# Kernel optimization log

Hardware: AMD Instinct MI355X
Metric: run time of the kernel (lower is better)

## Reference

```python
import jax, jax.numpy as jnp
import numpy as np


def setup_inputs() -> dict:
    key = jax.random.key(0)
    k1, k2 = jax.random.split(key)
    q_embed = jax.random.normal(k1, (1000, 1024), dtype=jnp.float32)      # (V, D)
    conv_feat = jax.random.normal(k2, (64, 1024, 800), dtype=jnp.float32)  # (B, D, T)
    return {"q_embed": q_embed, "conv_feat": conv_feat}


def reference(q_embed, conv_feat):
    # sim_scores: (B, V, T) = q_embed (V, D) @ conv_feat (B, D, T), no scaling
    sim_scores = jnp.einsum('vd,bdt->bvt', q_embed, conv_feat)
    attention_weights = jax.nn.softmax(sim_scores, axis=2)  # over T
    # context: (B, V, D) = weights (B, V, T) @ conv_feat^T (B, T, D)
    context_vector = jnp.einsum('bvt,bdt->bvd', attention_weights, conv_feat)
    return (context_vector, attention_weights)
```

## Files before the change

### kernel.cpp

```cpp
#include <hip/hip_runtime.h>
#include <hip/hip_bf16.h>

typedef short bf16x8 __attribute__((ext_vector_type(8)));
typedef float f32x4 __attribute__((ext_vector_type(4)));

#define NV 1000
#define ND 1024
#define NT 800
#define NB 64

__device__ inline unsigned short f32_bf16(float f) {
    unsigned u = __builtin_bit_cast(unsigned, f);
    return (unsigned short)((u + 0x7FFFu + ((u >> 16) & 1u)) >> 16);
}
__device__ inline void split_bf16(float f, unsigned short& h, unsigned short& l) {
    unsigned u = __builtin_bit_cast(unsigned, f);
    unsigned hb = (u + 0x7FFFu + ((u >> 16) & 1u)) >> 16;
    h = (unsigned short)hb;
    float hf = __builtin_bit_cast(float, hb << 16);
    float lf = f - hf;
    unsigned ul = __builtin_bit_cast(unsigned, lf);
    l = (unsigned short)((ul + 0x7FFFu + ((ul >> 16) & 1u)) >> 16);
}

__device__ inline void gload16(const void* g, void* l) {
    __builtin_amdgcn_global_load_lds(
        (const __attribute__((address_space(1))) unsigned int*)g,
        (__attribute__((address_space(3))) unsigned int*)l, 16, 0, 0);
}

__global__ __launch_bounds__(256) void prep_q(const float* __restrict__ Q,
                                              unsigned short* __restrict__ Qh,
                                              unsigned short* __restrict__ Ql) {
    int idx = blockIdx.x * 256 + threadIdx.x;
    int row = idx >> 8;
    int c4 = (idx & 255) << 2;
    float4 f = make_float4(0.f, 0.f, 0.f, 0.f);
    if (row < NV) f = *(const float4*)(Q + (size_t)row * ND + c4);
    unsigned short h0,h1,h2,h3,l0,l1,l2,l3;
    split_bf16(f.x,h0,l0); split_bf16(f.y,h1,l1);
    split_bf16(f.z,h2,l2); split_bf16(f.w,h3,l3);
    *(ushort4*)(Qh + (size_t)row * ND + c4) = make_ushort4(h0,h1,h2,h3);
    *(ushort4*)(Ql + (size_t)row * ND + c4) = make_ushort4(l0,l1,l2,l3);
}

__global__ __launch_bounds__(256) void prep_c(const float* __restrict__ C,
                                              unsigned short* __restrict__ Cth,
                                              unsigned short* __restrict__ Ctl,
                                              unsigned short* __restrict__ Cbf,
                                              int writeCbf) {
    const int dt = blockIdx.x;
    const int tt = blockIdx.y;
    const int b  = blockIdx.z;
    const int tid = threadIdx.x;
    __shared__ float T[64][33];
    const float* Cb = C + (size_t)b * ND * NT;
    const int d0 = dt * 64, t0 = tt * 32;
#pragma unroll
    for (int r = 0; r < 2; ++r) {
        int idx = r * 256 + tid;
        int row = idx >> 3;
        int c4 = (idx & 7) << 2;
        float4 f = *(const float4*)(Cb + (size_t)(d0 + row) * NT + t0 + c4);
        T[row][c4 + 0] = f.x; T[row][c4 + 1] = f.y;
        T[row][c4 + 2] = f.z; T[row][c4 + 3] = f.w;
        if (writeCbf) {
            *(ushort4*)(Cbf + ((size_t)b * ND + d0 + row) * NT + t0 + c4) =
                make_ushort4(f32_bf16(f.x), f32_bf16(f.y), f32_bf16(f.z), f32_bf16(f.w));
        }
    }
    __syncthreads();
#pragma unroll
    for (int r = 0; r < 2; ++r) {
        int idx = r * 256 + tid;
        int trow = idx >> 4;
        int dc = (idx & 15) << 2;
        unsigned short h[4], l[4];
#pragma unroll
        for (int j = 0; j < 4; ++j) split_bf16(T[dc + j][trow], h[j], l[j]);
        size_t o = ((size_t)b * NT + t0 + trow) * ND + d0 + dc;
        *(ushort4*)(Cth + o) = make_ushort4(h[0],h[1],h[2],h[3]);
        *(ushort4*)(Ctl + o) = make_ushort4(l[0],l[1],l[2],l[3]);
    }
}

__global__ __launch_bounds__(256) void gemm1_kernel(const unsigned short* __restrict__ Qh,
                                                    const unsigned short* __restrict__ Ql,
                                                    const unsigned short* __restrict__ Cth,
                                                    const unsigned short* __restrict__ Ctl,
                                                    float* __restrict__ S) {
    const int h = blockIdx.x;
    const int L = (h & 7) * 320 + (h >> 3);
    const int bm = L & 7;
    const int rest = L >> 3;
    const int bn = rest % 5;
    const int b  = rest / 5;

    const int tid = threadIdx.x;
    const int lane = tid & 63;
    const int w = tid >> 6;
    const int wr = w >> 1, wc = w & 1;

    __shared__ unsigned short lds[2][18432];

    const int v0 = bm * 128, t0 = bn * 160;
    const unsigned short* Agh = Qh + (size_t)v0 * ND;
    const unsigned short* Agl = Ql + (size_t)v0 * ND;
    const unsigned short* Bgh = Cth + ((size_t)b * NT + t0) * ND;
    const unsigned short* Bgl = Ctl + ((size_t)b * NT + t0) * ND;

    f32x4 acc[4][5];
#pragma unroll
    for (int i = 0; i < 4; ++i)
#pragma unroll
        for (int j = 0; j < 5; ++j) acc[i][j] = (f32x4){0.f, 0.f, 0.f, 0.f};

    const int srow = lane >> 2;
    const int sslot = lane & 3;
    const int swz = (sslot ^ (srow & 3) ^ ((srow >> 2) & 3)) << 3;
    const int g = lane >> 4, rl = lane & 15;
    const int sx = (g ^ (rl & 3) ^ ((rl >> 2) & 3)) << 4;

#define G1_STAGE(K0, BUF)                                                     \
    {                                                                         \
        unsigned short* Lb = lds[BUF];                                        \
        for (int i = w; i < 8; i += 4) {                                      \
            int row = i * 16 + srow;                                          \
            gload16(Agh + (size_t)row * ND + swz + (K0), Lb + i * 512);       \
            gload16(Agl + (size_t)row * ND + swz + (K0), Lb + 4096 + i * 512);\
        }                                                                     \
        for (int i = w; i < 10; i += 4) {                                     \
            int row = i * 16 + srow;                                          \
            gload16(Bgh + (size_t)row * ND + swz + (K0), Lb + 8192 + i * 512);\
            gload16(Bgl + (size_t)row * ND + swz + (K0), Lb + 13312 + i * 512);\
        }                                                                     \
    }

#define G1_COMPUTE(BUF)                                                       \
    {                                                                         \
        const char* Lb = (const char*)lds[BUF];                               \
        bf16x8 ah[4], al[4], bh[5], bl[5];                                    \
        _Pragma("unroll")                                                     \
        for (int mf = 0; mf < 4; ++mf) {                                      \
            int off = (wr * 64 + mf * 16 + rl) * 64 + sx;                     \
            ah[mf] = *(const bf16x8*)(Lb + off);                              \
            al[mf] = *(const bf16x8*)(Lb + 8192 + off);                       \
        }                                                                     \
        _Pragma("unroll")                                                     \
        for (int nf = 0; nf < 5; ++nf) {                                      \
            int off = (wc * 80 + nf * 16 + rl) * 64 + sx;                     \
            bh[nf] = *(const bf16x8*)(Lb + 16384 + off);                      \
            bl[nf] = *(const bf16x8*)(Lb + 26624 + off);                      \
        }                                                                     \
        _Pragma("unroll")                                                     \
        for (int mf = 0; mf < 4; ++mf)                                        \
            _Pragma("unroll")                                                 \
            for (int nf = 0; nf < 5; ++nf) {                                  \
                acc[mf][nf] = __builtin_amdgcn_mfma_f32_16x16x32_bf16(ah[mf], bh[nf], acc[mf][nf], 0, 0, 0); \
                acc[mf][nf] = __builtin_amdgcn_mfma_f32_16x16x32_bf16(ah[mf], bl[nf], acc[mf][nf], 0, 0, 0); \
                acc[mf][nf] = __builtin_amdgcn_mfma_f32_16x16x32_bf16(al[mf], bh[nf], acc[mf][nf], 0, 0, 0); \
            }                                                                 \
    }

    G1_STAGE(0, 0);
    __syncthreads();
    int cur = 0;
    for (int t = 0; t < 31; ++t) {
        G1_STAGE((t + 1) * 32, cur ^ 1);
        G1_COMPUTE(cur);
        __syncthreads();
        cur ^= 1;
    }
    G1_COMPUTE(cur);

    float* Sb = S + (size_t)b * NV * NT;
#pragma unroll
    for (int mf = 0; mf < 4; ++mf) {
#pragma unroll
        for (int nf = 0; nf < 5; ++nf) {
#pragma unroll
            for (int r = 0; r < 4; ++r) {
                int v = v0 + wr * 64 + mf * 16 + g * 4 + r;
                int t = t0 + wc * 80 + nf * 16 + rl;
                if (v < NV) Sb[(size_t)v * NT + t] = acc[mf][nf][r];
            }
        }
    }
#undef G1_STAGE
#undef G1_COMPUTE
}

__global__ __launch_bounds__(256) void softmax_kernel(float* __restrict__ S,
                                                      unsigned short* __restrict__ Wbf,
                                                      int writeWbf) {
    const int row = blockIdx.x * 4 + (threadIdx.x >> 6);
    const int lane = threadIdx.x & 63;
    float* p = S + (size_t)row * NT;
    unsigned short* pw = Wbf + (size_t)row * NT;
    float v[13];
    float m = -INFINITY;
#pragma unroll
    for (int i = 0; i < 13; ++i) {
        int t = i * 64 + lane;
        v[i] = (t < NT) ? p[t] : -INFINITY;
        m = fmaxf(m, v[i]);
    }
#pragma unroll
    for (int off = 32; off; off >>= 1) m = fmaxf(m, __shfl_xor(m, off));
    float s = 0.f;
#pragma unroll
    for (int i = 0; i < 13; ++i) {
        int t = i * 64 + lane;
        float e = (t < NT) ? __expf(v[i] - m) : 0.f;
        v[i] = e;
        s += e;
    }
#pragma unroll
    for (int off = 32; off; off >>= 1) s += __shfl_xor(s, off);
    const float inv = 1.0f / s;
#pragma unroll
    for (int i = 0; i < 13; ++i) {
        int t = i * 64 + lane;
        if (t < NT) {
            float wv = v[i] * inv;
            p[t] = wv;
            if (writeWbf) pw[t] = f32_bf16(wv);
        }
    }
}

__global__ __launch_bounds__(512) void gemm2_fast(const unsigned short* __restrict__ Wbf,
                                                  const unsigned short* __restrict__ Cbf,
                                                  float* __restrict__ O) {
    const int h = blockIdx.x;
    const int L = (h & 7) * 128 + (h >> 3);
    const int b  = L >> 4;
    const int bm = (L >> 2) & 3;
    const int bn = L & 3;
    const int tid = threadIdx.x;
    const int lane = tid & 63;
    const int w = tid >> 6;
    const int wr = w >> 2, wc = w & 3;

    __shared__ unsigned short lds[2][16384];

    const int v0 = bm * 256, d0 = bn * 256;
    const unsigned short* Ag = Wbf + (size_t)b * NV * NT;
    const unsigned short* Bg = Cbf + ((size_t)b * ND + d0) * NT;

    f32x4 acc[8][4];
#pragma unroll
    for (int i = 0; i < 8; ++i)
#pragma unroll
        for (int j = 0; j < 4; ++j) acc[i][j] = (f32x4){0.f, 0.f, 0.f, 0.f};

    const int srow = lane >> 2;
    const int sslot = lane & 3;
    const int swz = (sslot ^ (srow & 3) ^ ((srow >> 2) & 3)) << 3;
    const int g = lane >> 4, rl = lane & 15;
    const int sx = (g ^ (rl & 3) ^ ((rl >> 2) & 3)) << 4;

#define G2_STAGE(K0, BUF)                                                     \
    {                                                                         \
        unsigned short* Lb = lds[BUF];                                        \
        for (int i = w; i < 16; i += 8) {                                     \
            int row = i * 16 + srow;                                          \
            int vrow = v0 + row; if (vrow > NV - 1) vrow = NV - 1;            \
            gload16(Ag + (size_t)vrow * NT + swz + (K0), Lb + i * 512);       \
            gload16(Bg + (size_t)row * NT + swz + (K0), Lb + 8192 + i * 512); \
        }                                                                     \
    }

#define G2_COMPUTE(BUF)                                                       \
    {                                                                         \
        const char* Lb = (const char*)lds[BUF];                               \
        bf16x8 a[8], bq[4];                                                   \
        _Pragma("unroll")                                                     \
        for (int mf = 0; mf < 8; ++mf) {                                      \
            int off = (wr * 128 + mf * 16 + rl) * 64 + sx;                    \
            a[mf] = *(const bf16x8*)(Lb + off);                               \
        }                                                                     \
        _Pragma("unroll")                                                     \
        for (int nf = 0; nf < 4; ++nf) {                                      \
            int off = (wc * 64 + nf * 16 + rl) * 64 + sx;                     \
            bq[nf] = *(const bf16x8*)(Lb + 16384 + off);                      \
        }                                                                     \
        _Pragma("unroll")                                                     \
        for (int mf = 0; mf < 8; ++mf)                                        \
            _Pragma("unroll")                                                 \
            for (int nf = 0; nf < 4; ++nf)                                    \
                acc[mf][nf] = __builtin_amdgcn_mfma_f32_16x16x32_bf16(a[mf], bq[nf], acc[mf][nf], 0, 0, 0); \
    }

    G2_STAGE(0, 0);
    __syncthreads();
    int cur = 0;
    for (int t = 0; t < 24; ++t) {
        G2_STAGE((t + 1) * 32, cur ^ 1);
        G2_COMPUTE(cur);
        __syncthreads();
        cur ^= 1;
    }
    G2_COMPUTE(cur);

    float* Ob = O + (size_t)b * NV * ND;
#pragma unroll
    for (int mf = 0; mf < 8; ++mf) {
#pragma unroll
        for (int nf = 0; nf < 4; ++nf) {
#pragma unroll
            for (int r = 0; r < 4; ++r) {
                int v = v0 + wr * 128 + mf * 16 + g * 4 + r;
                int d = d0 + wc * 64 + nf * 16 + rl;
                if (v < NV) Ob[(size_t)v * ND + d] = acc[mf][nf][r];
            }
        }
    }
#undef G2_STAGE
#undef G2_COMPUTE
}

__global__ __launch_bounds__(256) void gemm2_mid(const unsigned short* __restrict__ Wbf,
                                                 const float* __restrict__ C,
                                                 float* __restrict__ O) {
    const int h = blockIdx.x;
    const int L = (h & 7) * 512 + (h >> 3);
    const int bm = L & 7;
    const int bn = (L >> 3) & 7;
    const int b  = L >> 6;
    const int tid = threadIdx.x;
    const int lane = tid & 63;
    const int w = tid >> 6;
    const int wr = w >> 1, wc = w & 1;

    __shared__ unsigned short As[128 * 32];
    __shared__ unsigned short Bs[128][40];

    const int v0 = bm * 128, d0 = bn * 128;
    const unsigned short* Ag = Wbf + (size_t)b * NV * NT;
    const float* Cb = C + (size_t)b * ND * NT;

    f32x4 acc[4][4];
#pragma unroll
    for (int i = 0; i < 4; ++i)
#pragma unroll
        for (int j = 0; j < 4; ++j) acc[i][j] = (f32x4){0.f, 0.f, 0.f, 0.f};

    const int srow = lane >> 2;
    const int sslot = lane & 3;

    for (int k0 = 0; k0 < NT; k0 += 32) {
        for (int i = w; i < 8; i += 4) {
            int row = i * 16 + srow;
            int c = ((sslot ^ (row & 3)) << 3) + k0;
            int vrow = v0 + row; if (vrow > NV - 1) vrow = NV - 1;
            gload16(Ag + (size_t)vrow * NT + c, As + i * 512);
        }
#pragma unroll
        for (int r = 0; r < 4; ++r) {
            int idx = r * 256 + tid;
            int row = idx >> 3;
            int kq  = (idx & 7) << 2;
            const float4 f = *(const float4*)(Cb + (size_t)(d0 + row) * NT + k0 + kq);
            *(ushort4*)&Bs[row][kq] = make_ushort4(f32_bf16(f.x), f32_bf16(f.y), f32_bf16(f.z), f32_bf16(f.w));
        }
        __syncthreads();

        const int g = lane >> 4, rl = lane & 15;
        const int sx = (g ^ (rl & 3)) << 4;
        const int kk = g << 3;
        bf16x8 a[4], bfr[4];
#pragma unroll
        for (int mf = 0; mf < 4; ++mf) {
            int off = (wr * 64 + mf * 16 + rl) * 64 + sx;
            a[mf] = *(const bf16x8*)((const char*)As + off);
        }
#pragma unroll
        for (int nf = 0; nf < 4; ++nf) {
            int row = wc * 64 + nf * 16 + rl;
            bfr[nf] = *(const bf16x8*)&Bs[row][kk];
        }
#pragma unroll
        for (int mf = 0; mf < 4; ++mf)
#pragma unroll
            for (int nf = 0; nf < 4; ++nf)
                acc[mf][nf] = __builtin_amdgcn_mfma_f32_16x16x32_bf16(a[mf], bfr[nf], acc[mf][nf], 0, 0, 0);
        __syncthreads();
    }

    float* Ob = O + (size_t)b * NV * ND;
    const int g = lane >> 4, rl = lane & 15;
#pragma unroll
    for (int mf = 0; mf < 4; ++mf) {
#pragma unroll
        for (int nf = 0; nf < 4; ++nf) {
#pragma unroll
            for (int r = 0; r < 4; ++r) {
                int v = v0 + wr * 64 + mf * 16 + g * 4 + r;
                int d = d0 + wc * 64 + nf * 16 + rl;
                if (v < NV) Ob[(size_t)v * ND + d] = acc[mf][nf][r];
            }
        }
    }
}

__global__ __launch_bounds__(256) void gemm2_slow(const float* __restrict__ W,
                                                  const float* __restrict__ C,
                                                  float* __restrict__ O) {
    const int h = blockIdx.x;
    const int L = (h & 7) * 512 + (h >> 3);
    const int bm = L & 7;
    const int bn = (L >> 3) & 7;
    const int b  = L >> 6;
    const int tid = threadIdx.x;
    const int lane = tid & 63;
    const int wid = tid >> 6;
    const int wr = wid >> 1;
    const int wc = wid & 1;

    __shared__ unsigned short As[128][40];
    __shared__ unsigned short Bs[128][40];

    const float* Wb = W + (size_t)b * NV * NT;
    const float* Cb = C + (size_t)b * ND * NT;
    const int v0 = bm * 128;
    const int d0 = bn * 128;

    f32x4 acc[4][4];
#pragma unroll
    for (int i = 0; i < 4; ++i)
#pragma unroll
        for (int j = 0; j < 4; ++j) acc[i][j] = (f32x4){0.f, 0.f, 0.f, 0.f};

    for (int k0 = 0; k0 < NT; k0 += 32) {
#pragma unroll
        for (int r = 0; r < 4; ++r) {
            int idx = r * 256 + tid;
            int row = idx >> 3;
            int kq  = (idx & 7) << 2;
            int v = v0 + row; if (v > NV - 1) v = NV - 1;
            const float4 f = *(const float4*)(Wb + (size_t)v * NT + k0 + kq);
            *(ushort4*)&As[row][kq] = make_ushort4(f32_bf16(f.x), f32_bf16(f.y), f32_bf16(f.z), f32_bf16(f.w));
        }
#pragma unroll
        for (int r = 0; r < 4; ++r) {
            int idx = r * 256 + tid;
            int row = idx >> 3;
            int kq  = (idx & 7) << 2;
            const float4 f = *(const float4*)(Cb + (size_t)(d0 + row) * NT + k0 + kq);
            *(ushort4*)&Bs[row][kq] = make_ushort4(f32_bf16(f.x), f32_bf16(f.y), f32_bf16(f.z), f32_bf16(f.w));
        }
        __syncthreads();

        bf16x8 a[4], bfr[4];
        const int kk = (lane >> 4) << 3;
#pragma unroll
        for (int mf = 0; mf < 4; ++mf) {
            int row = wr * 64 + mf * 16 + (lane & 15);
            a[mf] = *(const bf16x8*)&As[row][kk];
        }
#pragma unroll
        for (int nf = 0; nf < 4; ++nf) {
            int row = wc * 64 + nf * 16 + (lane & 15);
            bfr[nf] = *(const bf16x8*)&Bs[row][kk];
        }
#pragma unroll
        for (int mf = 0; mf < 4; ++mf)
#pragma unroll
            for (int nf = 0; nf < 4; ++nf)
                acc[mf][nf] = __builtin_amdgcn_mfma_f32_16x16x32_bf16(a[mf], bfr[nf], acc[mf][nf], 0, 0, 0);
        __syncthreads();
    }

    float* Ob = O + (size_t)b * NV * ND;
#pragma unroll
    for (int mf = 0; mf < 4; ++mf) {
#pragma unroll
        for (int nf = 0; nf < 4; ++nf) {
#pragma unroll
            for (int r = 0; r < 4; ++r) {
                int v = v0 + wr * 64 + mf * 16 + (lane >> 4) * 4 + r;
                int d = d0 + wc * 64 + nf * 16 + (lane & 15);
                if (v < NV) Ob[(size_t)v * ND + d] = acc[mf][nf][r];
            }
        }
    }
}

extern "C" void kernel_launch(void* const* d_in, const int* in_sizes, int n_in,
                              void* d_out, int out_size, void* d_ws, size_t ws_size,
                              hipStream_t stream) {
    const float* Q = (const float*)d_in[0];
    const float* C = (const float*)d_in[1];
    float* ctx = (float*)d_out;
    float* wts = ctx + (size_t)NB * NV * ND;

    unsigned short* Cth = (unsigned short*)ctx;
    unsigned short* Ctl = Cth + (size_t)NB * NT * ND;
    unsigned short* Qh  = Ctl + (size_t)NB * NT * ND;
    unsigned short* Ql  = Qh + (size_t)1024 * ND;

    const size_t WbfBytes = (size_t)NB * NV * NT * 2;
    const size_t CbfBytes = (size_t)NB * ND * NT * 2;
    unsigned short* Wbf = (unsigned short*)d_ws;
    unsigned short* Cbf = (unsigned short*)((char*)d_ws + WbfBytes);
    const int wsFast = ws_size >= WbfBytes + CbfBytes;
    const int wsMid  = ws_size >= WbfBytes;

    prep_q<<<dim3(1024), 256, 0, stream>>>(Q, Qh, Ql);
    prep_c<<<dim3(16, 25, NB), 256, 0, stream>>>(C, Cth, Ctl, Cbf, wsFast);
    gemm1_kernel<<<dim3(2560), 256, 0, stream>>>(Qh, Ql, Cth, Ctl, wts);
    softmax_kernel<<<dim3(16000), 256, 0, stream>>>(wts, Wbf, wsMid);
    if (wsFast)      gemm2_fast<<<dim3(1024), 512, 0, stream>>>(Wbf, Cbf, ctx);
    else if (wsMid)  gemm2_mid<<<dim3(4096), 256, 0, stream>>>(Wbf, C, ctx);
    else             gemm2_slow<<<dim3(4096), 256, 0, stream>>>(wts, C, ctx);
}
```

Measured before the change: 705.7 us.

## Use partial vmcnt waits so next-stage loads overlap compute in both GEMMs

Swaps the full __syncthreads after prefetch for explicit s_waitcnt vmcnt(N) plus s_barrier. Each wave waits only for the previous stage's global-to-LDS loads while the next stage's loads stay in flight during MFMA compute. GEMM1 staging is also rebalanced so each wave issues exactly 9 loads, which makes the vmcnt count exact. The risk is correctness: this depends on the loads being counted by vmcnt and on the exact number of loads issued per wave.

```diff
diff --git a/kernel.cpp b/kernel.cpp
--- a/kernel.cpp
+++ b/kernel.cpp
@@ -101,7 +101,7 @@
     const int w = tid >> 6;
     const int wr = w >> 1, wc = w & 1;
 
-    __shared__ unsigned short lds[2][18432];
+    __shared__ unsigned short lds[2 * 18432];
 
     const int v0 = bm * 128, t0 = bn * 160;
     const unsigned short* Agh = Qh + (size_t)v0 * ND;
@@ -121,24 +121,25 @@
     const int g = lane >> 4, rl = lane & 15;
     const int sx = (g ^ (rl & 3) ^ ((rl >> 2) & 3)) << 4;
 
-#define G1_STAGE(K0, BUF)                                                     \
-    {                                                                         \
-        unsigned short* Lb = lds[BUF];                                        \
-        for (int i = w; i < 8; i += 4) {                                      \
-            int row = i * 16 + srow;                                          \
-            gload16(Agh + (size_t)row * ND + swz + (K0), Lb + i * 512);       \
-            gload16(Agl + (size_t)row * ND + swz + (K0), Lb + 4096 + i * 512);\
-        }                                                                     \
-        for (int i = w; i < 10; i += 4) {                                     \
-            int row = i * 16 + srow;                                          \
-            gload16(Bgh + (size_t)row * ND + swz + (K0), Lb + 8192 + i * 512);\
-            gload16(Bgl + (size_t)row * ND + swz + (K0), Lb + 13312 + i * 512);\
-        }                                                                     \
+#define G1_STAGE(K0, BUF)                                                      \
+    {                                                                          \
+        unsigned short* Lb = lds + (BUF) * 18432;                              \
+        _Pragma("unroll")                                                      \
+        for (int j = 0; j < 9; ++j) {                                          \
+            int k = w * 9 + j;                                                 \
+            const unsigned short* src;                                         \
+            unsigned short* dst;                                               \
+            if (k < 8)       { src = Agh + (size_t)(k * 16 + srow) * ND;          dst = Lb + k * 512; }             \
+            else if (k < 16) { src = Agl + (size_t)((k - 8) * 16 + srow) * ND;    dst = Lb + 4096 + (k - 8) * 512; } \
+            else if (k < 26) { src = Bgh + (size_t)((k - 16) * 16 + srow) * ND;   dst = Lb + 8192 + (k - 16) * 512; } \
+            else             { src = Bgl + (size_t)((k - 26) * 16 + srow) * ND;   dst = Lb + 13312 + (k - 26) * 512; } \
+            gload16(src + swz + (K0), dst);                                    \
+        }                                                                      \
     }
 
 #define G1_COMPUTE(BUF)                                                       \
     {                                                                         \
-        const char* Lb = (const char*)lds[BUF];                               \
+        const char* Lb = (const char*)(lds + (BUF) * 18432);                  \
         bf16x8 ah[4], al[4], bh[5], bl[5];                                    \
         _Pragma("unroll")                                                     \
         for (int mf = 0; mf < 4; ++mf) {                                      \
@@ -163,14 +164,16 @@
     }
 
     G1_STAGE(0, 0);
-    __syncthreads();
     int cur = 0;
+#pragma unroll 1
     for (int t = 0; t < 31; ++t) {
         G1_STAGE((t + 1) * 32, cur ^ 1);
+        asm volatile("s_waitcnt vmcnt(9)\n\ts_barrier" ::: "memory");
         G1_COMPUTE(cur);
-        __syncthreads();
+        asm volatile("s_waitcnt lgkmcnt(0)\n\ts_barrier" ::: "memory");
         cur ^= 1;
     }
+    asm volatile("s_waitcnt vmcnt(0)\n\ts_barrier" ::: "memory");
     G1_COMPUTE(cur);
 
     float* Sb = S + (size_t)b * NV * NT;
@@ -242,7 +245,7 @@
     const int w = tid >> 6;
     const int wr = w >> 2, wc = w & 3;
 
-    __shared__ unsigned short lds[2][16384];
+    __shared__ unsigned short lds[2 * 16384];
 
     const int v0 = bm * 256, d0 = bn * 256;
     const unsigned short* Ag = Wbf + (size_t)b * NV * NT;
@@ -262,7 +265,8 @@
 
 #define G2_STAGE(K0, BUF)                                                     \
     {                                                                         \
-        unsigned short* Lb = lds[BUF];                                        \
+        unsigned short* Lb = lds + (BUF) * 16384;                             \
+        _Pragma("unroll")                                                     \
         for (int i = w; i < 16; i += 8) {                                     \
             int row = i * 16 + srow;                                          \
             int vrow = v0 + row; if (vrow > NV - 1) vrow = NV - 1;            \
@@ -273,7 +277,7 @@
 
 #define G2_COMPUTE(BUF)                                                       \
     {                                                                         \
-        const char* Lb = (const char*)lds[BUF];                               \
+        const char* Lb = (const char*)(lds + (BUF) * 16384);                  \
         bf16x8 a[8], bq[4];                                                   \
         _Pragma("unroll")                                                     \
         for (int mf = 0; mf < 8; ++mf) {                                      \
@@ -293,14 +297,16 @@
     }
 
     G2_STAGE(0, 0);
-    __syncthreads();
     int cur = 0;
+#pragma unroll 1
     for (int t = 0; t < 24; ++t) {
         G2_STAGE((t + 1) * 32, cur ^ 1);
+        asm volatile("s_waitcnt vmcnt(4)\n\ts_barrier" ::: "memory");
         G2_COMPUTE(cur);
-        __syncthreads();
+        asm volatile("s_waitcnt lgkmcnt(0)\n\ts_barrier" ::: "memory");
         cur ^= 1;
     }
+    asm volatile("s_waitcnt vmcnt(0)\n\ts_barrier" ::: "memory");
     G2_COMPUTE(cur);
 
     float* Ob = O + (size_t)b * NV * ND;
```

Result: slower. 824.0 us (+16.8%).
